# Kernel tuning notes

Measured on AMD Instinct MI355X. Metric: run time of the kernel, lower is better.

## Reference

```python
import jax, jax.numpy as jnp
import numpy as np

TEMPERATURE = 0.07
EPS = 1e-8  # torch F.cosine_similarity eps


def setup_inputs() -> dict:
    key = jax.random.key(0)
    k1, k2 = jax.random.split(key)
    N, D = 4096, 256
    z1 = jax.random.normal(k1, (N, D), dtype=jnp.float32)
    z2 = jax.random.normal(k2, (N, D), dtype=jnp.float32)
    return {"z1": z1, "z2": z2}


def reference(z1, z2):
    N = z1.shape[0]
    z = jnp.concatenate([z1, z2], axis=0)  # (2N, D)
    # cosine similarity = normalize(z) @ normalize(z).T (with eps clamp on norms)
    norms = jnp.maximum(jnp.linalg.norm(z, axis=-1, keepdims=True), EPS)
    zn = z / norms
    sim = (zn @ zn.T) / TEMPERATURE  # (2N, 2N)
    twoN = 2 * N
    eye = jnp.eye(twoN, dtype=bool)
    sim = jnp.where(eye, -1e9, sim)
    pos = jnp.concatenate([jnp.arange(N, twoN), jnp.arange(0, N)])
    # cross entropy with integer targets, mean reduction
    logZ = jax.nn.logsumexp(sim, axis=-1)  # (2N,)
    pos_logit = jnp.take_along_axis(sim, pos[:, None], axis=1)[:, 0]
    loss = jnp.mean(logZ - pos_logit)
    return loss
```

## Files before the change

kernel.cpp:

```cpp
#include <hip/hip_runtime.h>

#define N2   8192
#define DDIM 256
#define NBLK 64
#define NTRI 2080

static constexpr float INV_T = 1.0f / 0.07f;

using bf16x8 = __attribute__((ext_vector_type(8))) __bf16;
using f32x4  = __attribute__((ext_vector_type(4))) float;
using u16x4  = __attribute__((ext_vector_type(4))) unsigned short;
typedef unsigned short u16;
typedef unsigned int   u32;

#define GL2LDS(gp, lp) __builtin_amdgcn_global_load_lds( \
    (const __attribute__((address_space(1))) void*)(gp), \
    (__attribute__((address_space(3))) void*)(lp), 16, 0, 0)

__device__ __forceinline__ u16 f2bf(float f) {
    u32 u = __float_as_uint(f);
    u32 r = (u + 0x7fffu + ((u >> 16) & 1u)) >> 16;
    return (u16)r;
}

__global__ void ntx_norm(const float* __restrict__ z1, const float* __restrict__ z2,
                         u16* __restrict__ zn)
{
    const int w    = threadIdx.x >> 6;
    const int lane = threadIdx.x & 63;
    const int row  = blockIdx.x * 4 + w;

    const float* src = (row < 4096) ? (z1 + (size_t)row * DDIM)
                                    : (z2 + (size_t)(row - 4096) * DDIM);
    float4 v = *(const float4*)(src + lane * 4);
    float ss = v.x * v.x + v.y * v.y + v.z * v.z + v.w * v.w;
    #pragma unroll
    for (int m = 1; m < 64; m <<= 1) ss += __shfl_xor(ss, m, 64);

    float inv = 1.0f / fmaxf(sqrtf(ss), 1e-8f);

    u16x4 o;
    o.x = f2bf(v.x * inv); o.y = f2bf(v.y * inv);
    o.z = f2bf(v.z * inv); o.w = f2bf(v.w * inv);
    *(u16x4*)(zn + (size_t)row * DDIM + lane * 4) = o;
}

__global__ __launch_bounds__(256, 3)
void ntx_gemm(const u16* __restrict__ zn, float* __restrict__ partials,
              float* __restrict__ pos)
{
    __shared__ u16 lsA[8192];
    __shared__ u16 lsB[8192];

    const int tid  = threadIdx.x;
    const int lane = tid & 63;
    const int w    = tid >> 6;
    const int wr   = w >> 1;
    const int wc   = w & 1;

    const int t = (int)blockIdx.x;
    int br = (int)((129.0f - sqrtf(16641.0f - 8.0f * (float)t)) * 0.5f);
    while ((br + 1) * (129 - (br + 1)) / 2 <= t) ++br;
    while (br * (129 - br) / 2 > t) --br;
    const int bc = br + (t - br * (129 - br) / 2);

    const int fr  = lane & 15;
    const int kl  = lane >> 4;
    const int swz = (fr & 7) << 4;

    const int srow = w * 8 + (lane >> 3);
    const int scsw = ((lane & 7) * 16) ^ ((lane >> 3) << 4);

    auto stage = [&](int kt) {
        const char* gA = (const char*)zn + (size_t)(br * 128 + srow) * 512 + kt * 128 + scsw;
        const char* gB = (const char*)zn + (size_t)(bc * 128 + srow) * 512 + kt * 128 + scsw;
        u16* lA = &lsA[w * 512];
        u16* lB = &lsB[w * 512];
        #pragma unroll
        for (int i = 0; i < 4; ++i) {
            GL2LDS(gA + (size_t)i * 16384, lA + i * 2048);
            GL2LDS(gB + (size_t)i * 16384, lB + i * 2048);
        }
    };

    f32x4 acc[4][4] = {};

    stage(0);
    __syncthreads();

    #pragma unroll
    for (int kt = 0; kt < 4; ++kt) {
        #pragma unroll
        for (int ks = 0; ks < 2; ++ks) {
            const int kb = ks * 64 + kl * 16;
            bf16x8 af[4], bv[4];
            #pragma unroll
            for (int mf = 0; mf < 4; ++mf) {
                const int r = wr * 64 + mf * 16 + fr;
                af[mf] = *(const bf16x8*)((const char*)lsA + r * 128 + (kb ^ swz));
            }
            #pragma unroll
            for (int nf = 0; nf < 4; ++nf) {
                const int c = wc * 64 + nf * 16 + fr;
                bv[nf] = *(const bf16x8*)((const char*)lsB + c * 128 + (kb ^ swz));
            }
            #pragma unroll
            for (int mf = 0; mf < 4; ++mf)
                #pragma unroll
                for (int nf = 0; nf < 4; ++nf)
                    acc[mf][nf] = __builtin_amdgcn_mfma_f32_16x16x32_bf16(
                        af[mf], bv[nf], acc[mf][nf], 0, 0, 0);
        }
        if (kt < 3) {
            __syncthreads();
            stage(kt + 1);
            __syncthreads();
        }
    }

    const bool offdiag = (br != bc);
    const bool posblk  = (bc == br + 32);
    float colsum[4] = {0.f, 0.f, 0.f, 0.f};

    #pragma unroll
    for (int mf = 0; mf < 4; ++mf) {
        float rs[4] = {0.f, 0.f, 0.f, 0.f};
        const int rowq = br * 128 + wr * 64 + mf * 16 + kl * 4;
        #pragma unroll
        for (int nf = 0; nf < 4; ++nf) {
            const int col = bc * 128 + wc * 64 + nf * 16 + fr;
            f32x4 a = acc[mf][nf];
            #pragma unroll
            for (int j = 0; j < 4; ++j) {
                float e = (rowq + j == col) ? 0.f : __expf((a[j] - 1.0f) * INV_T);
                rs[j]      += e;
                colsum[nf] += e;
                if (posblk && (rowq + j + 4096 == col)) {
                    pos[rowq + j] = a[j];
                    pos[col]      = a[j];
                }
            }
        }
        #pragma unroll
        for (int m = 1; m < 16; m <<= 1) {
            #pragma unroll
            for (int j = 0; j < 4; ++j) rs[j] += __shfl_xor(rs[j], m, 64);
        }
        if (fr == 0) {
            float* p = partials + (size_t)rowq * 128 + bc * 2 + wc;
            p[0]   = rs[0];
            p[128] = rs[1];
            p[256] = rs[2];
            p[384] = rs[3];
        }
    }

    if (offdiag) {
        #pragma unroll
        for (int m = 16; m < 64; m <<= 1) {
            #pragma unroll
            for (int nf = 0; nf < 4; ++nf) colsum[nf] += __shfl_xor(colsum[nf], m, 64);
        }
        if (kl == 0) {
            #pragma unroll
            for (int nf = 0; nf < 4; ++nf) {
                const int col = bc * 128 + wc * 64 + nf * 16 + fr;
                partials[(size_t)col * 128 + br * 2 + wr] = colsum[nf];
            }
        }
    }
}

__global__ void ntx_loss(const float* __restrict__ partials, const float* __restrict__ pos,
                         float* __restrict__ loss)
{
    const int w    = threadIdx.x >> 6;
    const int lane = threadIdx.x & 63;
    const int row  = blockIdx.x * 4 + w;

    float S = partials[(size_t)row * 128 + lane] + partials[(size_t)row * 128 + 64 + lane];
    #pragma unroll
    for (int m = 1; m < 64; m <<= 1) S += __shfl_xor(S, m, 64);

    if (lane == 0)
        loss[row] = __logf(S) + INV_T - pos[row] * INV_T;
}

__global__ void ntx_reduce(const float* __restrict__ loss, float* __restrict__ out)
{
    __shared__ float sm[1024];
    const int t = threadIdx.x;
    float s = 0.f;
    for (int i = t; i < N2; i += 1024) s += loss[i];
    sm[t] = s;
    __syncthreads();
    for (int wdt = 512; wdt > 0; wdt >>= 1) {
        if (t < wdt) sm[t] += sm[t + wdt];
        __syncthreads();
    }
    if (t == 0) out[0] = sm[0] * (1.0f / (float)N2);
}

extern "C" void kernel_launch(void* const* d_in, const int* in_sizes, int n_in,
                              void* d_out, int out_size, void* d_ws, size_t ws_size,
                              hipStream_t stream)
{
    const float* z1 = (const float*)d_in[0];
    const float* z2 = (const float*)d_in[1];
    float* out = (float*)d_out;

    u16*   zn       = (u16*)d_ws;
    float* partials = (float*)((char*)d_ws + (4u << 20));
    float* loss     = (float*)((char*)d_ws + (8u << 20));
    float* pos      = loss + N2;

    ntx_norm  <<<N2 / 4, 256, 0, stream>>>(z1, z2, zn);
    ntx_gemm  <<<NTRI, 256, 0, stream>>>(zn, partials, pos);
    ntx_loss  <<<N2 / 4, 256, 0, stream>>>(partials, pos, loss);
    ntx_reduce<<<1, 1024, 0, stream>>>(loss, out);
}
```

Before: 47.79 us.

## Switch similarity GEMM to FP8 MFMA and fuse loss/reduce via last-block atomic

The normalized embeddings are now quantized to FP8 instead of BF16, and the GEMM uses fp8 MFMA with half the K-tile stages and setprio around the MFMA burst. The separate loss and reduce kernels are merged into one 64-block kernel that uses an atomic counter so the last block performs the final sum, with a memset to reset the counter. This cuts memory traffic, halves the k-loop iterations and removes one launch. In exchange FP8 precision for cosine similarities scaled by 1/0.07 may cause noticeable loss error.

```diff
diff --git a/kernel.cpp b/kernel.cpp
--- a/kernel.cpp
+++ b/kernel.cpp
@@ -2,29 +2,20 @@
 
 #define N2   8192
 #define DDIM 256
-#define NBLK 64
 #define NTRI 2080
 
 static constexpr float INV_T = 1.0f / 0.07f;
 
-using bf16x8 = __attribute__((ext_vector_type(8))) __bf16;
-using f32x4  = __attribute__((ext_vector_type(4))) float;
-using u16x4  = __attribute__((ext_vector_type(4))) unsigned short;
-typedef unsigned short u16;
-typedef unsigned int   u32;
+using f32x4 = __attribute__((ext_vector_type(4))) float;
+typedef unsigned int  u32;
+typedef long long     i64;
 
 #define GL2LDS(gp, lp) __builtin_amdgcn_global_load_lds( \
     (const __attribute__((address_space(1))) void*)(gp), \
     (__attribute__((address_space(3))) void*)(lp), 16, 0, 0)
 
-__device__ __forceinline__ u16 f2bf(float f) {
-    u32 u = __float_as_uint(f);
-    u32 r = (u + 0x7fffu + ((u >> 16) & 1u)) >> 16;
-    return (u16)r;
-}
-
 __global__ void ntx_norm(const float* __restrict__ z1, const float* __restrict__ z2,
-                         u16* __restrict__ zn)
+                         unsigned char* __restrict__ zn)
 {
     const int w    = threadIdx.x >> 6;
     const int lane = threadIdx.x & 63;
@@ -39,18 +30,17 @@
 
     float inv = 1.0f / fmaxf(sqrtf(ss), 1e-8f);
 
-    u16x4 o;
-    o.x = f2bf(v.x * inv); o.y = f2bf(v.y * inv);
-    o.z = f2bf(v.z * inv); o.w = f2bf(v.w * inv);
-    *(u16x4*)(zn + (size_t)row * DDIM + lane * 4) = o;
+    u32 p = __builtin_amdgcn_cvt_pk_fp8_f32(v.x * inv, v.y * inv, 0u, false);
+    p     = __builtin_amdgcn_cvt_pk_fp8_f32(v.z * inv, v.w * inv, p, true);
+    ((u32*)zn)[(size_t)row * 64 + lane] = p;
 }
 
 __global__ __launch_bounds__(256, 3)
-void ntx_gemm(const u16* __restrict__ zn, float* __restrict__ partials,
+void ntx_gemm(const unsigned char* __restrict__ zn, float* __restrict__ partials,
               float* __restrict__ pos)
 {
-    __shared__ u16 lsA[8192];
-    __shared__ u16 lsB[8192];
+    __shared__ unsigned char lsA[16384];
+    __shared__ unsigned char lsB[16384];
 
     const int tid  = threadIdx.x;
     const int lane = tid & 63;
@@ -66,57 +56,55 @@
 
     const int fr  = lane & 15;
     const int kl  = lane >> 4;
-    const int swz = (fr & 7) << 4;
-
-    const int srow = w * 8 + (lane >> 3);
-    const int scsw = ((lane & 7) * 16) ^ ((lane >> 3) << 4);
+    const int swz = (fr & 3) << 4;
 
     auto stage = [&](int kt) {
-        const char* gA = (const char*)zn + (size_t)(br * 128 + srow) * 512 + kt * 128 + scsw;
-        const char* gB = (const char*)zn + (size_t)(bc * 128 + srow) * 512 + kt * 128 + scsw;
-        u16* lA = &lsA[w * 512];
-        u16* lB = &lsB[w * 512];
         #pragma unroll
         for (int i = 0; i < 4; ++i) {
-            GL2LDS(gA + (size_t)i * 16384, lA + i * 2048);
-            GL2LDS(gB + (size_t)i * 16384, lB + i * 2048);
+            const int row = i * 32 + w * 8 + (lane >> 3);
+            const int sc  = ((lane & 7) * 16) ^ ((row & 3) << 4);
+            GL2LDS((const char*)zn + (size_t)(br * 128 + row) * 256 + kt * 128 + sc,
+                   (unsigned char*)lsA + i * 4096 + w * 1024);
+            GL2LDS((const char*)zn + (size_t)(bc * 128 + row) * 256 + kt * 128 + sc,
+                   (unsigned char*)lsB + i * 4096 + w * 1024);
         }
     };
 
     f32x4 acc[4][4] = {};
 
-    stage(0);
-    __syncthreads();
-
-    #pragma unroll
-    for (int kt = 0; kt < 4; ++kt) {
-        #pragma unroll
-        for (int ks = 0; ks < 2; ++ks) {
-            const int kb = ks * 64 + kl * 16;
-            bf16x8 af[4], bv[4];
+    auto compute = [&]() {
+        #pragma unroll
+        for (int ks = 0; ks < 4; ++ks) {
+            const int kb = ks * 32 + kl * 8;
+            i64 af[4], bv[4];
             #pragma unroll
             for (int mf = 0; mf < 4; ++mf) {
                 const int r = wr * 64 + mf * 16 + fr;
-                af[mf] = *(const bf16x8*)((const char*)lsA + r * 128 + (kb ^ swz));
+                af[mf] = *(const i64*)((const char*)lsA + r * 128 + (kb ^ swz));
             }
             #pragma unroll
             for (int nf = 0; nf < 4; ++nf) {
                 const int c = wc * 64 + nf * 16 + fr;
-                bv[nf] = *(const bf16x8*)((const char*)lsB + c * 128 + (kb ^ swz));
-            }
+                bv[nf] = *(const i64*)((const char*)lsB + c * 128 + (kb ^ swz));
+            }
+            __builtin_amdgcn_s_setprio(1);
             #pragma unroll
             for (int mf = 0; mf < 4; ++mf)
                 #pragma unroll
                 for (int nf = 0; nf < 4; ++nf)
-                    acc[mf][nf] = __builtin_amdgcn_mfma_f32_16x16x32_bf16(
+                    acc[mf][nf] = __builtin_amdgcn_mfma_f32_16x16x32_fp8_fp8(
                         af[mf], bv[nf], acc[mf][nf], 0, 0, 0);
-        }
-        if (kt < 3) {
-            __syncthreads();
-            stage(kt + 1);
-            __syncthreads();
-        }
-    }
+            __builtin_amdgcn_s_setprio(0);
+        }
+    };
+
+    stage(0);
+    __syncthreads();
+    compute();
+    __syncthreads();
+    stage(1);
+    __syncthreads();
+    compute();
 
     const bool offdiag = (br != bc);
     const bool posblk  = (bc == br + 32);
@@ -172,33 +160,45 @@
 }
 
 __global__ void ntx_loss(const float* __restrict__ partials, const float* __restrict__ pos,
-                         float* __restrict__ loss)
-{
-    const int w    = threadIdx.x >> 6;
-    const int lane = threadIdx.x & 63;
-    const int row  = blockIdx.x * 4 + w;
-
-    float S = partials[(size_t)row * 128 + lane] + partials[(size_t)row * 128 + 64 + lane];
+                         float* __restrict__ bsums, u32* __restrict__ counter,
+                         float* __restrict__ out)
+{
+    __shared__ float sm[16];
+    __shared__ u32 flag;
+    const int tid  = threadIdx.x;
+    const int lane = tid & 63;
+    const int w    = tid >> 6;
+
+    float a = 0.f;
     #pragma unroll
-    for (int m = 1; m < 64; m <<= 1) S += __shfl_xor(S, m, 64);
-
-    if (lane == 0)
-        loss[row] = __logf(S) + INV_T - pos[row] * INV_T;
-}
-
-__global__ void ntx_reduce(const float* __restrict__ loss, float* __restrict__ out)
-{
-    __shared__ float sm[1024];
-    const int t = threadIdx.x;
-    float s = 0.f;
-    for (int i = t; i < N2; i += 1024) s += loss[i];
-    sm[t] = s;
-    __syncthreads();
-    for (int wdt = 512; wdt > 0; wdt >>= 1) {
-        if (t < wdt) sm[t] += sm[t + wdt];
-        __syncthreads();
-    }
-    if (t == 0) out[0] = sm[0] * (1.0f / (float)N2);
+    for (int i = 0; i < 8; ++i) {
+        const int row = blockIdx.x * 128 + w * 8 + i;
+        float S = partials[(size_t)row * 128 + lane] + partials[(size_t)row * 128 + 64 + lane];
+        #pragma unroll
+        for (int m = 1; m < 64; m <<= 1) S += __shfl_xor(S, m, 64);
+        if (lane == 0) a += __logf(S) + INV_T - pos[row] * INV_T;
+    }
+    if (lane == 0) sm[w] = a;
+    __syncthreads();
+
+    if (tid == 0) {
+        float b = 0.f;
+        #pragma unroll
+        for (int i = 0; i < 16; ++i) b += sm[i];
+        bsums[blockIdx.x] = b;
+        __threadfence();
+        u32 old = atomicAdd(counter, 1u);
+        flag = (old == 63u) ? 1u : 0u;
+    }
+    __syncthreads();
+
+    if (flag && w == 0) {
+        __threadfence();
+        float v = bsums[lane];
+        #pragma unroll
+        for (int m = 1; m < 64; m <<= 1) v += __shfl_xor(v, m, 64);
+        if (lane == 0) out[0] = v * (1.0f / (float)N2);
+    }
 }
 
 extern "C" void kernel_launch(void* const* d_in, const int* in_sizes, int n_in,
@@ -209,13 +209,14 @@
     const float* z2 = (const float*)d_in[1];
     float* out = (float*)d_out;
 
-    u16*   zn       = (u16*)d_ws;
-    float* partials = (float*)((char*)d_ws + (4u << 20));
-    float* loss     = (float*)((char*)d_ws + (8u << 20));
-    float* pos      = loss + N2;
-
-    ntx_norm  <<<N2 / 4, 256, 0, stream>>>(z1, z2, zn);
-    ntx_gemm  <<<NTRI, 256, 0, stream>>>(zn, partials, pos);
-    ntx_loss  <<<N2 / 4, 256, 0, stream>>>(partials, pos, loss);
-    ntx_reduce<<<1, 1024, 0, stream>>>(loss, out);
-}
+    unsigned char* zn       = (unsigned char*)d_ws;
+    float*         partials = (float*)((char*)d_ws + (2u << 20));
+    float*         pos      = (float*)((char*)d_ws + (6u << 20));
+    float*         bsums    = pos + N2;
+    u32*           counter  = (u32*)(bsums + 64);
+
+    hipMemsetAsync(counter, 0, 4, stream);
+    ntx_norm<<<N2 / 4, 256, 0, stream>>>(z1, z2, zn);
+    ntx_gemm<<<NTRI, 256, 0, stream>>>(zn, partials, pos);
+    ntx_loss<<<64, 1024, 0, stream>>>(partials, pos, bsums, counter, out);
+}
```

Result: slower. 55.21 us (+15.5%).
